# Kernel tuning notes

Measured on AMD Instinct MI355X. Metric: run time of the kernel, lower is better.

The kernel has to match this reference:

```python
import jax, jax.numpy as jnp
import numpy as np

HEADS = 16
DIM_HEAD = 64
DIM = 1024
INNER = HEADS * DIM_HEAD  # 1024


def setup_inputs() -> dict:
    key = jax.random.key(0)
    ks = jax.random.split(key, 8)
    B, N, M = 4, 2048, 2048
    x = jax.random.normal(ks[0], (B, N, DIM), dtype=jnp.float32)
    context = jax.random.normal(ks[1], (B, M, DIM), dtype=jnp.float32)
    x_mask = (jax.random.uniform(ks[2], (B, N)) > 0.1).astype(jnp.float32)
    context_mask = (jax.random.uniform(ks[3], (B, M)) > 0.1).astype(jnp.float32)
    s = 0.02
    Wq = jax.random.normal(ks[4], (DIM, INNER), dtype=jnp.float32) * s
    Wkv = jax.random.normal(ks[5], (DIM, 2 * INNER), dtype=jnp.float32) * s
    Wo = jax.random.normal(ks[6], (INNER, DIM), dtype=jnp.float32) * s
    bo = jnp.zeros((DIM,), dtype=jnp.float32)
    return {"x": x, "context": context, "x_mask": x_mask,
            "context_mask": context_mask, "Wq": Wq, "Wkv": Wkv, "Wo": Wo, "bo": bo}


def _split_heads(t):
    b, n, _ = t.shape
    return t.reshape(b, n, HEADS, DIM_HEAD).transpose(0, 2, 1, 3)  # b h n d


def reference(x, context, x_mask, context_mask, Wq, Wkv, Wo, bo):
    scale = DIM_HEAD ** -0.5
    q = _split_heads(x @ Wq)                       # b h n d
    kv = context @ Wkv
    k = _split_heads(kv[..., :INNER])              # b h m d
    v = _split_heads(kv[..., INNER:])              # b h m d
    dots = jnp.einsum('bhnd,bhmd->bhnm', q, k) * scale
    # attn_bias = 1 - x_mask ⊗ context_mask; masked where isclose(attn_bias, 1)
    prod = x_mask[:, None, :, None] * context_mask[:, None, None, :]  # b 1 n m
    masked = jnp.isclose(1.0 - prod, 1.0)          # b 1 n m, broadcast over heads
    dots = jnp.where(masked, -jnp.inf, dots)       # b h n m
    # rows with no valid key: zero the whole row before softmax
    valid = jnp.any(~masked, axis=-1, keepdims=True)  # b 1 n 1
    dots = jnp.where(valid, dots, 0.0)
    attn = jax.nn.softmax(dots, axis=-1)
    attn = jnp.where(valid, attn, 0.0)
    out = jnp.einsum('bhnm,bhmd->bhnd', attn, v)
    b, h, n, d = out.shape
    out = out.transpose(0, 2, 1, 3).reshape(b, n, h * d)
    return out @ Wo + bo
```

## Files before the change

### kernel.cpp

```cpp
#include <hip/hip_runtime.h>

#define DEVI __device__ __forceinline__

typedef __attribute__((ext_vector_type(4))) float f32x4;
typedef __attribute__((ext_vector_type(8))) _Float16 f16x8;
typedef __attribute__((ext_vector_type(2))) _Float16 f16x2;

#if __has_builtin(__builtin_amdgcn_exp2f)
#define EXP2F __builtin_amdgcn_exp2f
#else
#define EXP2F exp2f
#endif

DEVI ushort f2h(float f) {
  _Float16 h = (_Float16)f;
  return __builtin_bit_cast(ushort, h);
}

DEVI unsigned pkrtz(float a, float b) {
  return __builtin_bit_cast(unsigned, __builtin_amdgcn_cvt_pkrtz(a, b));
}

DEVI float dot2acc(unsigned pk, float acc) {
#if __has_builtin(__builtin_amdgcn_fdot2)
  f16x2 one2 = {(_Float16)1.0f, (_Float16)1.0f};
  return __builtin_amdgcn_fdot2(__builtin_bit_cast(f16x2, pk), one2, acc, false);
#else
  f16x2 v = __builtin_bit_cast(f16x2, pk);
  return acc + (float)v[0] + (float)v[1];
#endif
}

DEVI void gload_lds16(const void* g, void* l) {
  typedef const unsigned int GlobU __attribute__((address_space(1)));
  typedef unsigned int LdsU __attribute__((address_space(3)));
  __builtin_amdgcn_global_load_lds((GlobU*)g, (LdsU*)l, 16, 0, 0);
}

__global__ __launch_bounds__(256) void cast_f16_kernel(
    const float4* __restrict__ x, const float4* __restrict__ ctx,
    ushort4* __restrict__ xo, ushort4* __restrict__ co) {
  int i = blockIdx.x * 256 + threadIdx.x;
  const float4* src;
  ushort4* dst;
  int j;
  if (i < 2097152) { src = x; dst = xo; j = i; }
  else             { src = ctx; dst = co; j = i - 2097152; }
  float4 v = src[j];
  ushort4 o;
  o.x = f2h(v.x); o.y = f2h(v.y); o.z = f2h(v.z); o.w = f2h(v.w);
  dst[j] = o;
}

__global__ __launch_bounds__(256) void transpose_cast_kernel(
    const float* __restrict__ Wq, const float* __restrict__ Wkv,
    const float* __restrict__ Wo, ushort* __restrict__ WqT,
    ushort* __restrict__ WkvT, ushort* __restrict__ WoT) {
  __shared__ ushort tile[64][65];
  int bx = blockIdx.x;
  const float* in; ushort* out; int C, cb;
  if (bx < 16)      { in = Wq;  out = WqT;  C = 1024; cb = bx * 64; }
  else if (bx < 48) { in = Wkv; out = WkvT; C = 2048; cb = (bx - 16) * 64; }
  else              { in = Wo;  out = WoT;  C = 1024; cb = (bx - 48) * 64; }
  const int R = 1024;
  int rb = blockIdx.y * 64;
  int t = threadIdx.x;
  int c4 = (t & 15) * 4, r0 = t >> 4;
#pragma unroll
  for (int i = 0; i < 4; i++) {
    int r = r0 + i * 16;
    float4 v = *(const float4*)(in + (size_t)(rb + r) * C + cb + c4);
    tile[r][c4 + 0] = f2h(v.x);
    tile[r][c4 + 1] = f2h(v.y);
    tile[r][c4 + 2] = f2h(v.z);
    tile[r][c4 + 3] = f2h(v.w);
  }
  __syncthreads();
#pragma unroll
  for (int i = 0; i < 4; i++) {
    int rr = r0 + i * 16;
    ushort4 o;
    o.x = tile[c4 + 0][rr]; o.y = tile[c4 + 1][rr];
    o.z = tile[c4 + 2][rr]; o.w = tile[c4 + 3][rr];
    *(ushort4*)(out + (size_t)(cb + rr) * R + rb + c4) = o;
  }
}

DEVI void gemm_core(const ushort* __restrict__ A, const ushort* __restrict__ Bt,
                    int K, int rowbase, int colbase, int tid,
                    ushort* As, ushort* Bs, f32x4 acc[4][4]) {
  const int lane = tid & 63, wave = tid >> 6;
  const int quad = lane >> 4, ln = lane & 15;
  const int wrow = (wave >> 1) * 64, wcol = (wave & 1) * 64;
  for (int k0 = 0; k0 < K; k0 += 32) {
    __syncthreads();
#pragma unroll
    for (int i = 0; i < 2; i++) {
      int f = i * 256 + tid;
      int r = f >> 2;
      int c = (f & 3) ^ (r & 3);
      gload_lds16(A + (size_t)(rowbase + r) * K + (k0 + c * 8),
                  (char*)As + (size_t)(i * 256 + wave * 64) * 16);
      gload_lds16(Bt + (size_t)(colbase + r) * K + (k0 + c * 8),
                  (char*)Bs + (size_t)(i * 256 + wave * 64) * 16);
    }
    __syncthreads();
    f16x8 a[4], b[4];
#pragma unroll
    for (int mt = 0; mt < 4; mt++) {
      int r = wrow + mt * 16 + ln;
      a[mt] = *(const f16x8*)(As + ((size_t)r * 4 + (quad ^ (r & 3))) * 8);
    }
#pragma unroll
    for (int nt = 0; nt < 4; nt++) {
      int r = wcol + nt * 16 + ln;
      b[nt] = *(const f16x8*)(Bs + ((size_t)r * 4 + (quad ^ (r & 3))) * 8);
    }
#pragma unroll
    for (int mt = 0; mt < 4; mt++)
#pragma unroll
      for (int nt = 0; nt < 4; nt++)
        acc[mt][nt] = __builtin_amdgcn_mfma_f32_16x16x32_f16(a[mt], b[nt], acc[mt][nt], 0, 0, 0);
  }
}

__global__ __launch_bounds__(256, 2) void qkv_gemm(
    const ushort* __restrict__ xb, const ushort* __restrict__ cb,
    const ushort* __restrict__ WqT, const ushort* __restrict__ WkvT,
    ushort* __restrict__ Qo, ushort* __restrict__ Ko, ushort* __restrict__ Vo) {
  __shared__ ushort As[128 * 32];
  __shared__ ushort Bs[128 * 32];
  const int tid = threadIdx.x;
  const int lane = tid & 63, wave = tid >> 6;
  const int quad = lane >> 4, ln = lane & 15;
  const int cy = blockIdx.y;
  const bool isQ = cy < 8;
  const int colbase = (isQ ? cy : cy - 8) * 128;
  const int rowbase = blockIdx.x * 128;
  const int wrow = (wave >> 1) * 64, wcol = (wave & 1) * 64;
  f32x4 acc[4][4] = {};
  gemm_core(isQ ? xb : cb, isQ ? WqT : WkvT, 1024, rowbase, colbase, tid, As, Bs, acc);

  if (isQ) {
    const float qscale = 0.18033688011112042f;
#pragma unroll
    for (int nt = 0; nt < 4; nt++) {
      int col = colbase + wcol + nt * 16 + ln;
      int h = col >> 6, d = col & 63;
#pragma unroll
      for (int mt = 0; mt < 4; mt++) {
        int row = rowbase + wrow + mt * 16 + quad * 4;
#pragma unroll
        for (int r = 0; r < 4; r++) {
          int rr = row + r;
          int bb = rr >> 11, n = rr & 2047;
          Qo[(((size_t)bb * 16 + h) * 2048 + n) * 64 + d] = f2h(acc[mt][nt][r] * qscale);
        }
      }
    }
  } else {
    bool isK = (colbase < 1024);
#pragma unroll
    for (int nt = 0; nt < 4; nt++) {
      int col = colbase + wcol + nt * 16 + ln;
#pragma unroll
      for (int mt = 0; mt < 4; mt++) {
        int row = rowbase + wrow + mt * 16 + quad * 4;
        int bb = row >> 11, m = row & 2047;
        if (isK) {
          int h = col >> 6, d = col & 63;
#pragma unroll
          for (int r = 0; r < 4; r++)
            Ko[(((size_t)bb * 16 + h) * 2048 + (m + r)) * 64 + d] = f2h(acc[mt][nt][r]);
        } else {
          int c2 = col - 1024;
          int h = c2 >> 6, d = c2 & 63;
          uint2 pv;
          pv.x = pkrtz(acc[mt][nt][0], acc[mt][nt][1]);
          pv.y = pkrtz(acc[mt][nt][2], acc[mt][nt][3]);
          *(uint2*)(Vo + (((size_t)bb * 16 + h) * 64 + d) * 2048 + m) = pv;
        }
      }
    }
  }
}

__global__ __launch_bounds__(256, 2) void out_gemm(
    const ushort* __restrict__ A, const ushort* __restrict__ Bt,
    float* __restrict__ C, const float* __restrict__ bias) {
  __shared__ ushort As[128 * 32];
  __shared__ ushort Bs[128 * 32];
  const int tid = threadIdx.x;
  const int lane = tid & 63, wave = tid >> 6;
  const int quad = lane >> 4, ln = lane & 15;
  const int colbase = blockIdx.y * 128, rowbase = blockIdx.x * 128;
  const int wrow = (wave >> 1) * 64, wcol = (wave & 1) * 64;
  f32x4 acc[4][4] = {};
  gemm_core(A, Bt, 1024, rowbase, colbase, tid, As, Bs, acc);
#pragma unroll
  for (int nt = 0; nt < 4; nt++) {
    int col = colbase + wcol + nt * 16 + ln;
    float bv = bias[col];
#pragma unroll
    for (int mt = 0; mt < 4; mt++) {
      int row = rowbase + wrow + mt * 16 + quad * 4;
#pragma unroll
      for (int r = 0; r < 4; r++)
        C[(size_t)(row + r) * 1024 + col] = acc[mt][nt][r] + bv;
    }
  }
}

__global__ __launch_bounds__(512, 4) void attn_kernel(
    const ushort* __restrict__ Q, const ushort* __restrict__ K,
    const ushort* __restrict__ VT, const float* __restrict__ xmask,
    const float* __restrict__ cmask, ushort* __restrict__ O) {
  __shared__ ushort Ks[2][64 * 64];
  __shared__ ushort Vs[2][64 * 64];
  __shared__ ushort Ps[8 * 32 * 40];
  __shared__ float CMB[2048];
  const int tid = threadIdx.x, lane = tid & 63, wave = tid >> 6;
  const int quad = lane >> 4, ln = lane & 15;
  const int bid = blockIdx.x;
  const int qb = bid >> 6, bh6 = bid & 63, h = bh6 & 15, b = bh6 >> 4;
  const size_t bh = (size_t)b * 16 + h;
  const ushort* Qbh = Q + bh * (2048 * 64);
  const ushort* Kbh = K + bh * (2048 * 64);
  const ushort* Vbh = VT + bh * (64 * 2048);
  const int q0 = qb * 256 + wave * 32;

  {
    float4 c0 = *(const float4*)(cmask + b * 2048 + tid * 4);
    float4 b0;
    b0.x = fmaf(c0.x, 3.0e4f, -3.0e4f); b0.y = fmaf(c0.y, 3.0e4f, -3.0e4f);
    b0.z = fmaf(c0.z, 3.0e4f, -3.0e4f); b0.w = fmaf(c0.w, 3.0e4f, -3.0e4f);
    *(float4*)(CMB + tid * 4) = b0;
  }

  f16x8 qf[2][2];
#pragma unroll
  for (int qt = 0; qt < 2; qt++)
#pragma unroll
    for (int kc = 0; kc < 2; kc++)
      qf[qt][kc] = *(const f16x8*)(Qbh + (size_t)(q0 + qt * 16 + ln) * 64 + kc * 32 + quad * 8);

  float xm[2];
#pragma unroll
  for (int qt = 0; qt < 2; qt++) xm[qt] = xmask[b * 2048 + q0 + qt * 16 + ln];

  __syncthreads();

  {
    int r = tid >> 3;
    int c = (tid & 7) ^ (r & 7);
#pragma unroll
    for (int t = 0; t < 2; t++) {
      gload_lds16(Kbh + (size_t)(t * 64 + r) * 64 + c * 8, (char*)Ks[t] + (size_t)tid * 16);
      gload_lds16(Vbh + (size_t)r * 2048 + (t * 64 + c * 8), (char*)Vs[t] + (size_t)tid * 16);
    }
  }

  f32x4 o[4][2] = {};
  float lpart[2] = {0.f, 0.f};

  for (int kb = 0; kb < 32; kb++) {
    const int cur = kb & 1;
    const int m0 = kb * 64;
    const ushort* KsC = Ks[cur];
    const ushort* VsC = Vs[cur];

    if (kb < 31) asm volatile("s_waitcnt vmcnt(2)" ::: "memory");
    else         asm volatile("s_waitcnt vmcnt(0)" ::: "memory");
    asm volatile("s_barrier" ::: "memory");

    f32x4 bias4[4];
#pragma unroll
    for (int kt = 0; kt < 4; kt++)
      bias4[kt] = *(const f32x4*)(CMB + m0 + kt * 16 + quad * 4);

    f32x4 s[4][2];
#pragma unroll
    for (int kt = 0; kt < 4; kt++)
#pragma unroll
      for (int qt = 0; qt < 2; qt++) s[kt][qt] = bias4[kt];
#pragma unroll
    for (int kc = 0; kc < 2; kc++) {
#pragma unroll
      for (int kt = 0; kt < 4; kt++) {
        int r = kt * 16 + ln;
        f16x8 ka = *(const f16x8*)(KsC + ((size_t)r * 8 + ((kc * 4 + quad) ^ (r & 7))) * 8);
#pragma unroll
        for (int qt = 0; qt < 2; qt++)
          s[kt][qt] = __builtin_amdgcn_mfma_f32_16x16x32_f16(ka, qf[qt][kc], s[kt][qt], 0, 0, 0);
      }
    }

#pragma unroll
    for (int kc = 0; kc < 2; kc++) {
#pragma unroll
      for (int qt = 0; qt < 2; qt++) {
        int qrow = qt * 16 + ln;
        ushort* pb = Ps + wave * (32 * 40) + qrow * 40;
#pragma unroll
        for (int t = 0; t < 2; t++) {
          int kt = kc * 2 + t;
          float p0 = EXP2F(s[kt][qt][0]);
          float p1 = EXP2F(s[kt][qt][1]);
          float p2 = EXP2F(s[kt][qt][2]);
          float p3 = EXP2F(s[kt][qt][3]);
          uint2 pv;
          pv.x = pkrtz(p0, p1);
          pv.y = pkrtz(p2, p3);
          lpart[qt] = dot2acc(pv.x, lpart[qt]);
          lpart[qt] = dot2acc(pv.y, lpart[qt]);
          *(uint2*)(pb + (t * 4 + quad) * 4) = pv;
        }
      }
      f16x8 pf[2];
#pragma unroll
      for (int qt = 0; qt < 2; qt++) {
        int qrow = qt * 16 + ln;
        pf[qt] = *(const f16x8*)(Ps + wave * (32 * 40) + qrow * 40 + quad * 8);
      }
#pragma unroll
      for (int dt = 0; dt < 4; dt++) {
        int r = dt * 16 + ln;
        f16x8 va = *(const f16x8*)(VsC + ((size_t)r * 8 + ((kc * 4 + quad) ^ (r & 7))) * 8);
#pragma unroll
        for (int qt = 0; qt < 2; qt++)
          o[dt][qt] = __builtin_amdgcn_mfma_f32_16x16x32_f16(va, pf[qt], o[dt][qt], 0, 0, 0);
      }
    }

    asm volatile("s_barrier" ::: "memory");
    if (kb < 30) {
      const int m2 = m0 + 128;
      int r = tid >> 3;
      int c = (tid & 7) ^ (r & 7);
      gload_lds16(Kbh + (size_t)(m2 + r) * 64 + c * 8, (char*)Ks[cur] + (size_t)tid * 16);
      gload_lds16(Vbh + (size_t)r * 2048 + (m2 + c * 8), (char*)Vs[cur] + (size_t)tid * 16);
    }
  }

#pragma unroll
  for (int qt = 0; qt < 2; qt++) {
    float l = lpart[qt];
    l += __shfl_xor(l, 16, 64);
    l += __shfl_xor(l, 32, 64);
    float inv = (xm[qt] != 0.f && l > 0.f) ? (1.f / l) : 0.f;
    int n = q0 + qt * 16 + ln;
    ushort* ob = O + ((size_t)(b * 2048 + n) * 16 + h) * 64;
#pragma unroll
    for (int dt = 0; dt < 4; dt++) {
      uint2 pv;
      pv.x = pkrtz(o[dt][qt][0] * inv, o[dt][qt][1] * inv);
      pv.y = pkrtz(o[dt][qt][2] * inv, o[dt][qt][3] * inv);
      *(uint2*)(ob + dt * 16 + quad * 4) = pv;
    }
  }
}

extern "C" void kernel_launch(void* const* d_in, const int* in_sizes, int n_in,
                              void* d_out, int out_size, void* d_ws, size_t ws_size,
                              hipStream_t stream) {
  const float* x   = (const float*)d_in[0];
  const float* ctx = (const float*)d_in[1];
  const float* xm  = (const float*)d_in[2];
  const float* cm  = (const float*)d_in[3];
  const float* Wq  = (const float*)d_in[4];
  const float* Wkv = (const float*)d_in[5];
  const float* Wo  = (const float*)d_in[6];
  const float* bo  = (const float*)d_in[7];

  char* ws = (char*)d_ws;
  const size_t MB = 1024 * 1024;
  ushort* xb   = (ushort*)(ws + 0);
  ushort* cb   = (ushort*)(ws + 16 * MB);
  ushort* WqT  = (ushort*)(ws + 32 * MB);
  ushort* WkvT = (ushort*)(ws + 34 * MB);
  ushort* WoT  = (ushort*)(ws + 38 * MB);
  ushort* Qb   = (ushort*)(ws + 40 * MB);
  ushort* Kb   = (ushort*)(ws + 56 * MB);
  ushort* VTb  = (ushort*)(ws + 72 * MB);
  ushort* Ob   = xb;

  cast_f16_kernel<<<16384, 256, 0, stream>>>((const float4*)x, (const float4*)ctx,
                                             (ushort4*)xb, (ushort4*)cb);
  transpose_cast_kernel<<<dim3(64, 16), 256, 0, stream>>>(Wq, Wkv, Wo, WqT, WkvT, WoT);
  qkv_gemm<<<dim3(64, 24), 256, 0, stream>>>(xb, cb, WqT, WkvT, Qb, Kb, VTb);
  attn_kernel<<<512, 512, 0, stream>>>(Qb, Kb, VTb, xm, cm, Ob);
  out_gemm<<<dim3(64, 8), 256, 0, stream>>>(Ob, WoT, (float*)d_out, bo);
}
```

Baseline: 313.4 us.

## Double-buffer GEMM LDS loads and store Q transposed for packed writes

The GEMM core moves to a two-stage LDS double buffer: the next tile is prefetched while MFMAs run on the current one, and waits use vmcnt counters plus raw barriers instead of two __syncthreads per step. Occupancy hints rise to 3 blocks. Q is now written transposed (d-major) with packed 4-element stores. The attention kernel then gathers Q fragments with scalar strided loads, and the P LDS layout is rearranged. The strided Q gather and the larger LDS footprint could offset part of the gain.

```diff
diff --git a/kernel.cpp b/kernel.cpp
--- a/kernel.cpp
+++ b/kernel.cpp
@@ -86,50 +86,69 @@
   }
 }
 
+DEVI void gemm_stage(const ushort* __restrict__ A, const ushort* __restrict__ Bt,
+                     int K, int rowbase, int colbase, int tid, int wave,
+                     ushort* AsC, ushort* BsC, int kk) {
+#pragma unroll
+  for (int i = 0; i < 2; i++) {
+    int f = i * 256 + tid;
+    int r = f >> 2;
+    int c = (f & 3) ^ (r & 3);
+    gload_lds16(A + (size_t)(rowbase + r) * K + (kk + c * 8),
+                (char*)AsC + (size_t)(i * 256 + wave * 64) * 16);
+    gload_lds16(Bt + (size_t)(colbase + r) * K + (kk + c * 8),
+                (char*)BsC + (size_t)(i * 256 + wave * 64) * 16);
+  }
+}
+
 DEVI void gemm_core(const ushort* __restrict__ A, const ushort* __restrict__ Bt,
-                    int K, int rowbase, int colbase, int tid,
+                    const int K, int rowbase, int colbase, int tid,
                     ushort* As, ushort* Bs, f32x4 acc[4][4]) {
   const int lane = tid & 63, wave = tid >> 6;
   const int quad = lane >> 4, ln = lane & 15;
   const int wrow = (wave >> 1) * 64, wcol = (wave & 1) * 64;
+
+  gemm_stage(A, Bt, K, rowbase, colbase, tid, wave, As, Bs, 0);
+  gemm_stage(A, Bt, K, rowbase, colbase, tid, wave, As + 4096, Bs + 4096, 32);
+
   for (int k0 = 0; k0 < K; k0 += 32) {
-    __syncthreads();
-#pragma unroll
-    for (int i = 0; i < 2; i++) {
-      int f = i * 256 + tid;
-      int r = f >> 2;
-      int c = (f & 3) ^ (r & 3);
-      gload_lds16(A + (size_t)(rowbase + r) * K + (k0 + c * 8),
-                  (char*)As + (size_t)(i * 256 + wave * 64) * 16);
-      gload_lds16(Bt + (size_t)(colbase + r) * K + (k0 + c * 8),
-                  (char*)Bs + (size_t)(i * 256 + wave * 64) * 16);
-    }
-    __syncthreads();
+    const int cur = (k0 >> 5) & 1;
+    ushort* AsC = As + cur * 4096;
+    ushort* BsC = Bs + cur * 4096;
+
+    if (k0 + 32 < K) asm volatile("s_waitcnt vmcnt(4)" ::: "memory");
+    else             asm volatile("s_waitcnt vmcnt(0)" ::: "memory");
+    asm volatile("s_barrier" ::: "memory");
+
     f16x8 a[4], b[4];
 #pragma unroll
     for (int mt = 0; mt < 4; mt++) {
       int r = wrow + mt * 16 + ln;
-      a[mt] = *(const f16x8*)(As + ((size_t)r * 4 + (quad ^ (r & 3))) * 8);
+      a[mt] = *(const f16x8*)(AsC + ((size_t)r * 4 + (quad ^ (r & 3))) * 8);
     }
 #pragma unroll
     for (int nt = 0; nt < 4; nt++) {
       int r = wcol + nt * 16 + ln;
-      b[nt] = *(const f16x8*)(Bs + ((size_t)r * 4 + (quad ^ (r & 3))) * 8);
+      b[nt] = *(const f16x8*)(BsC + ((size_t)r * 4 + (quad ^ (r & 3))) * 8);
     }
 #pragma unroll
     for (int mt = 0; mt < 4; mt++)
 #pragma unroll
       for (int nt = 0; nt < 4; nt++)
         acc[mt][nt] = __builtin_amdgcn_mfma_f32_16x16x32_f16(a[mt], b[nt], acc[mt][nt], 0, 0, 0);
-  }
-}
-
-__global__ __launch_bounds__(256, 2) void qkv_gemm(
+
+    asm volatile("s_barrier" ::: "memory");
+    if (k0 + 64 < K)
+      gemm_stage(A, Bt, K, rowbase, colbase, tid, wave, AsC, BsC, k0 + 64);
+  }
+}
+
+__global__ __launch_bounds__(256, 3) void qkv_gemm(
     const ushort* __restrict__ xb, const ushort* __restrict__ cb,
     const ushort* __restrict__ WqT, const ushort* __restrict__ WkvT,
     ushort* __restrict__ Qo, ushort* __restrict__ Ko, ushort* __restrict__ Vo) {
-  __shared__ ushort As[128 * 32];
-  __shared__ ushort Bs[128 * 32];
+  __shared__ ushort As[2 * 128 * 32];
+  __shared__ ushort Bs[2 * 128 * 32];
   const int tid = threadIdx.x;
   const int lane = tid & 63, wave = tid >> 6;
   const int quad = lane >> 4, ln = lane & 15;
@@ -142,7 +161,7 @@
   gemm_core(isQ ? xb : cb, isQ ? WqT : WkvT, 1024, rowbase, colbase, tid, As, Bs, acc);
 
   if (isQ) {
-    const float qscale = 0.18033688011112042f;
+    const float qs = 0.18033688011112042f;
 #pragma unroll
     for (int nt = 0; nt < 4; nt++) {
       int col = colbase + wcol + nt * 16 + ln;
@@ -150,12 +169,11 @@
 #pragma unroll
       for (int mt = 0; mt < 4; mt++) {
         int row = rowbase + wrow + mt * 16 + quad * 4;
-#pragma unroll
-        for (int r = 0; r < 4; r++) {
-          int rr = row + r;
-          int bb = rr >> 11, n = rr & 2047;
-          Qo[(((size_t)bb * 16 + h) * 2048 + n) * 64 + d] = f2h(acc[mt][nt][r] * qscale);
-        }
+        int bb = row >> 11, n = row & 2047;
+        uint2 pv;
+        pv.x = pkrtz(acc[mt][nt][0] * qs, acc[mt][nt][1] * qs);
+        pv.y = pkrtz(acc[mt][nt][2] * qs, acc[mt][nt][3] * qs);
+        *(uint2*)(Qo + (((size_t)bb * 16 + h) * 64 + d) * 2048 + n) = pv;
       }
     }
   } else {
@@ -185,11 +203,11 @@
   }
 }
 
-__global__ __launch_bounds__(256, 2) void out_gemm(
+__global__ __launch_bounds__(256, 3) void out_gemm(
     const ushort* __restrict__ A, const ushort* __restrict__ Bt,
     float* __restrict__ C, const float* __restrict__ bias) {
-  __shared__ ushort As[128 * 32];
-  __shared__ ushort Bs[128 * 32];
+  __shared__ ushort As[2 * 128 * 32];
+  __shared__ ushort Bs[2 * 128 * 32];
   const int tid = threadIdx.x;
   const int lane = tid & 63, wave = tid >> 6;
   const int quad = lane >> 4, ln = lane & 15;
@@ -212,19 +230,19 @@
 }
 
 __global__ __launch_bounds__(512, 4) void attn_kernel(
-    const ushort* __restrict__ Q, const ushort* __restrict__ K,
+    const ushort* __restrict__ QT, const ushort* __restrict__ K,
     const ushort* __restrict__ VT, const float* __restrict__ xmask,
     const float* __restrict__ cmask, ushort* __restrict__ O) {
   __shared__ ushort Ks[2][64 * 64];
   __shared__ ushort Vs[2][64 * 64];
-  __shared__ ushort Ps[8 * 32 * 40];
+  __shared__ ushort Ps[8 * 2048];
   __shared__ float CMB[2048];
   const int tid = threadIdx.x, lane = tid & 63, wave = tid >> 6;
   const int quad = lane >> 4, ln = lane & 15;
   const int bid = blockIdx.x;
   const int qb = bid >> 6, bh6 = bid & 63, h = bh6 & 15, b = bh6 >> 4;
   const size_t bh = (size_t)b * 16 + h;
-  const ushort* Qbh = Q + bh * (2048 * 64);
+  const ushort* QTbh = QT + bh * (64 * 2048);
   const ushort* Kbh = K + bh * (2048 * 64);
   const ushort* Vbh = VT + bh * (64 * 2048);
   const int q0 = qb * 256 + wave * 32;
@@ -241,8 +259,13 @@
 #pragma unroll
   for (int qt = 0; qt < 2; qt++)
 #pragma unroll
-    for (int kc = 0; kc < 2; kc++)
-      qf[qt][kc] = *(const f16x8*)(Qbh + (size_t)(q0 + qt * 16 + ln) * 64 + kc * 32 + quad * 8);
+    for (int kc = 0; kc < 2; kc++) {
+      int q = q0 + qt * 16 + ln;
+#pragma unroll
+      for (int j = 0; j < 8; j++)
+        qf[qt][kc][j] = __builtin_bit_cast(_Float16,
+            (unsigned short)QTbh[(size_t)(kc * 32 + quad * 8 + j) * 2048 + q]);
+    }
 
   float xm[2];
 #pragma unroll
@@ -299,8 +322,7 @@
     for (int kc = 0; kc < 2; kc++) {
 #pragma unroll
       for (int qt = 0; qt < 2; qt++) {
-        int qrow = qt * 16 + ln;
-        ushort* pb = Ps + wave * (32 * 40) + qrow * 40;
+        ushort* pb = Ps + wave * 2048 + (qt * 2 + kc) * 512;
 #pragma unroll
         for (int t = 0; t < 2; t++) {
           int kt = kc * 2 + t;
@@ -313,15 +335,13 @@
           pv.y = pkrtz(p2, p3);
           lpart[qt] = dot2acc(pv.x, lpart[qt]);
           lpart[qt] = dot2acc(pv.y, lpart[qt]);
-          *(uint2*)(pb + (t * 4 + quad) * 4) = pv;
+          *(uint2*)(pb + (t * 2 + (quad >> 1)) * 128 + ln * 8 + (quad & 1) * 4) = pv;
         }
       }
       f16x8 pf[2];
 #pragma unroll
-      for (int qt = 0; qt < 2; qt++) {
-        int qrow = qt * 16 + ln;
-        pf[qt] = *(const f16x8*)(Ps + wave * (32 * 40) + qrow * 40 + quad * 8);
-      }
+      for (int qt = 0; qt < 2; qt++)
+        pf[qt] = *(const f16x8*)(Ps + wave * 2048 + (qt * 2 + kc) * 512 + quad * 128 + ln * 8);
 #pragma unroll
       for (int dt = 0; dt < 4; dt++) {
         int r = dt * 16 + ln;
@@ -379,7 +399,7 @@
   ushort* WqT  = (ushort*)(ws + 32 * MB);
   ushort* WkvT = (ushort*)(ws + 34 * MB);
   ushort* WoT  = (ushort*)(ws + 38 * MB);
-  ushort* Qb   = (ushort*)(ws + 40 * MB);
+  ushort* QTb  = (ushort*)(ws + 40 * MB);
   ushort* Kb   = (ushort*)(ws + 56 * MB);
   ushort* VTb  = (ushort*)(ws + 72 * MB);
   ushort* Ob   = xb;
@@ -387,7 +407,7 @@
   cast_f16_kernel<<<16384, 256, 0, stream>>>((const float4*)x, (const float4*)ctx,
                                              (ushort4*)xb, (ushort4*)cb);
   transpose_cast_kernel<<<dim3(64, 16), 256, 0, stream>>>(Wq, Wkv, Wo, WqT, WkvT, WoT);
-  qkv_gemm<<<dim3(64, 24), 256, 0, stream>>>(xb, cb, WqT, WkvT, Qb, Kb, VTb);
-  attn_kernel<<<512, 512, 0, stream>>>(Qb, Kb, VTb, xm, cm, Ob);
+  qkv_gemm<<<dim3(64, 24), 256, 0, stream>>>(xb, cb, WqT, WkvT, QTb, Kb, VTb);
+  attn_kernel<<<512, 512, 0, stream>>>(QTb, Kb, VTb, xm, cm, Ob);
   out_gemm<<<dim3(64, 8), 256, 0, stream>>>(Ob, WoT, (float*)d_out, bo);
 }
```

Measured after the change: 299.1 us. 1.05x faster.
